# Kernel optimization log

Measured on AMD Instinct MI355X. Metric: run time of the kernel, lower is better.

The kernel has to match this reference:

```python
import jax, jax.numpy as jnp
import numpy as np

N_NODES = 50000
N_EDGES = 1600000
D = 128


def setup_inputs() -> dict:
    key = jax.random.key(0)
    k1, k2, k3, k4 = jax.random.split(key, 4)
    x = jax.random.normal(k1, (N_NODES, D), dtype=jnp.float32)
    edge_index = jax.random.randint(k2, (2, N_EDGES), 0, N_NODES, dtype=jnp.int64)
    # Xavier-uniform-like W; B is zeros in torch init but use small random for grad coverage
    limit = float(np.sqrt(6.0 / (D + D)))
    W = jax.random.uniform(k3, (D, D), dtype=jnp.float32, minval=-limit, maxval=limit)
    B = jax.random.uniform(k4, (D, D), dtype=jnp.float32, minval=-limit, maxval=limit)
    return {"x": x, "edge_index": edge_index, "W": W, "B": B}


def reference(x, edge_index, W, B):
    sources = edge_index[0]
    destinations = edge_index[1]
    # gather messages from source nodes, scatter-add into destinations
    messages = x[sources]  # [E, D]
    aggregated = jax.ops.segment_sum(messages, destinations, num_segments=N_NODES)  # [N, D]
    deg = jax.ops.segment_sum(jnp.ones((N_EDGES,), dtype=x.dtype), destinations, num_segments=N_NODES)
    deg = jnp.where(deg == 0, jnp.asarray(1.0, dtype=x.dtype), deg)
    mean_msg = aggregated / deg[:, None]
    # update: messages @ W.T + x @ B.T
    return mean_msg @ W.T + x @ B.T
```

## Files before the change

kernel.cpp:

```cpp
#include <hip/hip_runtime.h>
#include <hip/hip_bf16.h>

#define NN 50000
#define NE 1600000
#define DD 128
#define NPB 64
#define NBK 782
#define MAXB 2560
#define CHUNK 6144
#define NCB 261
#define WS 136

typedef __attribute__((ext_vector_type(8))) short short8;
typedef __attribute__((ext_vector_type(4))) float f32x4;

__device__ inline unsigned short to_bf16(float v) {
    __hip_bfloat16 h = __float2bfloat16(v);
    return __builtin_bit_cast(unsigned short, h);
}

__global__ __launch_bounds__(1024) void convscatter_k(const int* __restrict__ ei,
                                                      const float* __restrict__ x,
                                                      unsigned int* __restrict__ xb,
                                                      int* __restrict__ gcursor,
                                                      int* __restrict__ ebuf) {
    __shared__ int stg[CHUNK];
    __shared__ int h[NBK];
    __shared__ int lbase[NBK];
    __shared__ int gb[NBK];
    __shared__ int hcur[NBK];
    __shared__ int wsum[16], wbase[16];
    const int t = threadIdx.x;
    const int lane = t & 63, wv = t >> 6;
    const int e0 = blockIdx.x * CHUNK;
    const int ec = min(CHUNK, NE - e0);

    for (int i = t; i < NBK; i += 1024) h[i] = 0;
    __syncthreads();

    unsigned int w2[6];
    #pragma unroll
    for (int u = 0; u < 6; ++u) {
        int i = u * 1024 + t;
        if (i < ec) {
            int src = ei[e0 + i];
            int dst = ei[NE + e0 + i];
            int b = dst >> 6;
            w2[u] = ((unsigned)b << 22) | ((unsigned)src << 6) | (unsigned)(dst & 63);
            atomicAdd(&h[b], 1);
        } else w2[u] = 0xFFFFFFFFu;
    }

    {
        int gid = blockIdx.x * 1024 + t;
        const int total4 = NN * DD / 4;
        for (int i = gid; i < total4; i += NCB * 1024) {
            float4 v = ((const float4*)x)[i];
            int p = __builtin_amdgcn_cvt_pk_fp8_f32(v.x, v.y, 0, false);
            p = __builtin_amdgcn_cvt_pk_fp8_f32(v.z, v.w, p, true);
            xb[i] = (unsigned)p;
        }
    }
    __syncthreads();

    int v = (t < NBK) ? h[t] : 0;
    int s = v;
    #pragma unroll
    for (int o = 1; o < 64; o <<= 1) {
        int u = __shfl_up(s, o);
        if (lane >= o) s += u;
    }
    if (lane == 63) wsum[wv] = s;
    __syncthreads();
    if (wv == 0 && lane < 16) {
        int bv = wsum[lane];
        int bs = bv;
        #pragma unroll
        for (int o = 1; o < 16; o <<= 1) {
            int u = __shfl_up(bs, o);
            if (lane >= o) bs += u;
        }
        wbase[lane] = bs - bv;
    }
    __syncthreads();
    if (t < NBK) {
        int excl = s - v + wbase[wv];
        lbase[t] = excl;
        hcur[t] = excl;
        gb[t] = v ? t * MAXB + atomicAdd(&gcursor[t], v) : 0;
    }
    __syncthreads();

    #pragma unroll
    for (int u = 0; u < 6; ++u) {
        if (w2[u] != 0xFFFFFFFFu) {
            int b = w2[u] >> 22;
            int pos = atomicAdd(&hcur[b], 1);
            stg[pos] = (int)w2[u];
        }
    }
    __syncthreads();

    for (int i = t; i < ec; i += 1024) {
        unsigned int w = (unsigned)stg[i];
        int b = w >> 22;
        ebuf[gb[b] + (i - lbase[b])] = (int)(w & 0x3FFFFFu);
    }
}

__global__ __launch_bounds__(512) void sortagg_k(const unsigned int* __restrict__ xb,
                                                 const int* __restrict__ ebuf,
                                                 const int* __restrict__ gcursor,
                                                 unsigned int* __restrict__ meanb) {
    __shared__ int stg[MAXB];
    __shared__ unsigned short srt[MAXB];
    __shared__ int cnt8[8][NPB];
    __shared__ int cur[NPB], off[NPB + 1];
    const int b = blockIdx.x, t = threadIdx.x;
    const int wv = t >> 6, lane = t & 63;
    const int n = gcursor[b];
    const int* __restrict__ slab = ebuf + (size_t)b * MAXB;
    for (int i = t; i < n; i += 512) stg[i] = slab[i];
    if (lane < NPB) cnt8[wv][lane] = 0;
    __syncthreads();
    for (int i = t; i < n; i += 512) atomicAdd(&cnt8[wv][stg[i] & 63], 1);
    __syncthreads();
    if (t < 64) {
        int v = 0;
        #pragma unroll
        for (int w = 0; w < 8; ++w) v += cnt8[w][t];
        int s = v;
        #pragma unroll
        for (int o = 1; o < 64; o <<= 1) {
            int u = __shfl_up(s, o);
            if (t >= o) s += u;
        }
        cur[t] = s - v;
        off[t] = s - v;
        if (t == 63) off[64] = s;
    }
    __syncthreads();
    for (int i = t; i < n; i += 512) {
        int w = stg[i];
        int pos = atomicAdd(&cur[w & 63], 1);
        srt[pos] = (unsigned short)(w >> 6);
    }
    __syncthreads();

    const int half = lane >> 5, il = lane & 31;
    #pragma unroll
    for (int q = 0; q < 8; ++q) {
        int ln = wv + q * 8;
        int s0 = off[ln], s1 = off[ln + 1];
        float a0 = 0.f, a1 = 0.f, a2 = 0.f, a3 = 0.f;
        int i = s0;
        for (; i + 32 <= s1; i += 32) {
            unsigned int u[16];
            #pragma unroll
            for (int k = 0; k < 16; ++k)
                u[k] = xb[(size_t)srt[i + 2 * k + half] * 32 + il];
            #pragma unroll
            for (int k = 0; k < 16; ++k) {
                auto lo = __builtin_amdgcn_cvt_pk_f32_fp8((int)u[k], false);
                auto hi = __builtin_amdgcn_cvt_pk_f32_fp8((int)u[k], true);
                a0 += lo[0]; a1 += lo[1]; a2 += hi[0]; a3 += hi[1];
            }
        }
        if (i + 16 <= s1) {
            unsigned int u[8];
            #pragma unroll
            for (int k = 0; k < 8; ++k)
                u[k] = xb[(size_t)srt[i + 2 * k + half] * 32 + il];
            #pragma unroll
            for (int k = 0; k < 8; ++k) {
                auto lo = __builtin_amdgcn_cvt_pk_f32_fp8((int)u[k], false);
                auto hi = __builtin_amdgcn_cvt_pk_f32_fp8((int)u[k], true);
                a0 += lo[0]; a1 += lo[1]; a2 += hi[0]; a3 += hi[1];
            }
            i += 16;
        }
        for (; i < s1; i += 2) {
            int e = i + half;
            unsigned int u = (e < s1) ? xb[(size_t)srt[e] * 32 + il] : 0u;
            auto lo = __builtin_amdgcn_cvt_pk_f32_fp8((int)u, false);
            auto hi = __builtin_amdgcn_cvt_pk_f32_fp8((int)u, true);
            a0 += lo[0]; a1 += lo[1]; a2 += hi[0]; a3 += hi[1];
        }
        a0 += __shfl_xor(a0, 32);
        a1 += __shfl_xor(a1, 32);
        a2 += __shfl_xor(a2, 32);
        a3 += __shfl_xor(a3, 32);
        int node = b * NPB + ln;
        if (half == 0 && node < NN) {
            float inv = 1.0f / fmaxf((float)(s1 - s0), 1.0f);
            unsigned lo = (unsigned)to_bf16(a0 * inv) | ((unsigned)to_bf16(a1 * inv) << 16);
            unsigned hi = (unsigned)to_bf16(a2 * inv) | ((unsigned)to_bf16(a3 * inv) << 16);
            ((uint2*)meanb)[(size_t)node * 32 + il] = make_uint2(lo, hi);
        }
    }
}

__global__ __launch_bounds__(256) void gemm_mfma_k(const unsigned short* __restrict__ meanb,
                                                   const float* __restrict__ x,
                                                   const float* __restrict__ W,
                                                   const float* __restrict__ Bm,
                                                   float* __restrict__ out) {
    __shared__ unsigned short Wt[DD * WS];
    __shared__ unsigned short Bt[DD * WS];
    const int tid = threadIdx.x;
    #pragma unroll
    for (int it = 0; it < 16; ++it) {
        int idx = it * 256 + tid;
        int n = idx >> 5;
        int k0 = (idx & 31) * 4;
        float4 w4 = ((const float4*)W)[idx];
        float4 b4 = ((const float4*)Bm)[idx];
        ushort4 wp, bp;
        wp.x = to_bf16(w4.x); wp.y = to_bf16(w4.y); wp.z = to_bf16(w4.z); wp.w = to_bf16(w4.w);
        bp.x = to_bf16(b4.x); bp.y = to_bf16(b4.y); bp.z = to_bf16(b4.z); bp.w = to_bf16(b4.w);
        *(ushort4*)&Wt[n * WS + k0] = wp;
        *(ushort4*)&Bt[n * WS + k0] = bp;
    }
    __syncthreads();

    const int wave = tid >> 6;
    const int lane = tid & 63;
    const int m = lane & 15;
    const int quad = lane >> 4;
    const int rowA = min(blockIdx.x * 64 + wave * 16 + m, NN - 1);

    f32x4 acc[8];
    #pragma unroll
    for (int nt = 0; nt < 8; ++nt) acc[nt] = (f32x4){0.f, 0.f, 0.f, 0.f};

    #pragma unroll
    for (int t = 0; t < 4; ++t) {
        const int k8 = t * 32 + quad * 8;
        short8 mf = *(const short8*)&meanb[(size_t)rowA * DD + k8];
        float xv[8];
        {
            const float4* xq = (const float4*)&x[(size_t)rowA * DD + k8];
            float4 b0 = xq[0], b1 = xq[1];
            xv[0] = b0.x; xv[1] = b0.y; xv[2] = b0.z; xv[3] = b0.w;
            xv[4] = b1.x; xv[5] = b1.y; xv[6] = b1.z; xv[7] = b1.w;
        }
        short8 xh, xl;
        #pragma unroll
        for (int j = 0; j < 8; ++j) {
            unsigned short g = to_bf16(xv[j]);
            xh[j] = (short)g;
            xl[j] = (short)to_bf16(xv[j] - __uint_as_float((unsigned)g << 16));
        }
        #pragma unroll
        for (int nt = 0; nt < 8; ++nt) {
            int nrow = nt * 16 + m;
            short8 wf = *(const short8*)&Wt[nrow * WS + k8];
            short8 bf = *(const short8*)&Bt[nrow * WS + k8];
            acc[nt] = __builtin_amdgcn_mfma_f32_16x16x32_bf16(xl, bf, acc[nt], 0, 0, 0);
            acc[nt] = __builtin_amdgcn_mfma_f32_16x16x32_bf16(mf, wf, acc[nt], 0, 0, 0);
            acc[nt] = __builtin_amdgcn_mfma_f32_16x16x32_bf16(xh, bf, acc[nt], 0, 0, 0);
        }
    }

    const int rowD0 = blockIdx.x * 64 + wave * 16 + quad * 4;
    #pragma unroll
    for (int nt = 0; nt < 8; ++nt) {
        #pragma unroll
        for (int r = 0; r < 4; ++r) {
            int row = rowD0 + r;
            if (row < NN) out[(size_t)row * DD + nt * 16 + m] = acc[nt][r];
        }
    }
}

extern "C" void kernel_launch(void* const* d_in, const int* in_sizes, int n_in,
                              void* d_out, int out_size, void* d_ws, size_t ws_size,
                              hipStream_t stream) {
    const float* x  = (const float*)d_in[0];
    const int*   ei = (const int*)d_in[1];
    const float* W  = (const float*)d_in[2];
    const float* Bm = (const float*)d_in[3];
    float* out = (float*)d_out;

    unsigned int* meanb = (unsigned int*)d_ws;
    unsigned int* xb    = meanb + (size_t)NN * 64;
    int* ebuf     = (int*)(xb + (size_t)NN * 32);
    int* gcursor  = ebuf + (size_t)NBK * MAXB;

    hipMemsetAsync(gcursor, 0, NBK * sizeof(int), stream);
    convscatter_k<<<NCB, 1024, 0, stream>>>(ei, x, xb, gcursor, ebuf);
    sortagg_k<<<NBK, 512, 0, stream>>>(xb, ebuf, gcursor, meanb);
    gemm_mfma_k<<<(NN + 63) / 64, 256, 0, stream>>>((const unsigned short*)meanb, x, W, Bm, out);
}
```

Baseline: 154.0 us.

## Fuse mean aggregation with MFMA GEMM and precompute bf16 weights in scatter

Merges the aggregation and GEMM kernels so each 64-node block keeps its bf16 mean rows in shared memory and runs the MFMA update directly, removing the meanb global round trip and one launch. W and B are converted to bf16 once in the scatter kernel and read from global (L2) by the fused kernel instead of each GEMM block converting them into LDS. The scatter kernel is retuned to 512 blocks of 512 threads with 2 buckets per thread in the scan, and the 32-edge unrolled gather loop is dropped. Risks include more LDS per block in the fused kernel lowering occupancy, and B/W fragment loads from global instead of LDS.

Measured after the change: 177.5 us. 15.3% more time.

```diff
diff --git a/kernel.cpp b/kernel.cpp
--- a/kernel.cpp
+++ b/kernel.cpp
@@ -7,9 +7,9 @@
 #define NPB 64
 #define NBK 782
 #define MAXB 2560
-#define CHUNK 6144
-#define NCB 261
-#define WS 136
+#define CHUNK 3125
+#define NCB 512
+#define MS 136
 
 typedef __attribute__((ext_vector_type(8))) short short8;
 typedef __attribute__((ext_vector_type(4))) float f32x4;
@@ -19,30 +19,33 @@
     return __builtin_bit_cast(unsigned short, h);
 }
 
-__global__ __launch_bounds__(1024) void convscatter_k(const int* __restrict__ ei,
-                                                      const float* __restrict__ x,
-                                                      unsigned int* __restrict__ xb,
-                                                      int* __restrict__ gcursor,
-                                                      int* __restrict__ ebuf) {
+__global__ __launch_bounds__(512) void convscatter_k(const int* __restrict__ ei,
+                                                     const float* __restrict__ x,
+                                                     const float* __restrict__ W,
+                                                     const float* __restrict__ Bm,
+                                                     unsigned int* __restrict__ xb,
+                                                     unsigned int* __restrict__ Wb,
+                                                     unsigned int* __restrict__ Bb,
+                                                     int* __restrict__ gcursor,
+                                                     int* __restrict__ ebuf) {
     __shared__ int stg[CHUNK];
     __shared__ int h[NBK];
     __shared__ int lbase[NBK];
     __shared__ int gb[NBK];
     __shared__ int hcur[NBK];
-    __shared__ int wsum[16], wbase[16];
+    __shared__ int wsum[8], wbase[8];
     const int t = threadIdx.x;
     const int lane = t & 63, wv = t >> 6;
     const int e0 = blockIdx.x * CHUNK;
-    const int ec = min(CHUNK, NE - e0);
-
-    for (int i = t; i < NBK; i += 1024) h[i] = 0;
-    __syncthreads();
-
-    unsigned int w2[6];
-    #pragma unroll
-    for (int u = 0; u < 6; ++u) {
-        int i = u * 1024 + t;
-        if (i < ec) {
+
+    for (int i = t; i < NBK; i += 512) h[i] = 0;
+    __syncthreads();
+
+    unsigned int w2[7];
+    #pragma unroll
+    for (int u = 0; u < 7; ++u) {
+        int i = u * 512 + t;
+        if (i < CHUNK) {
             int src = ei[e0 + i];
             int dst = ei[NE + e0 + i];
             int b = dst >> 6;
@@ -52,19 +55,30 @@
     }
 
     {
-        int gid = blockIdx.x * 1024 + t;
+        int gid = blockIdx.x * 512 + t;
         const int total4 = NN * DD / 4;
-        for (int i = gid; i < total4; i += NCB * 1024) {
+        for (int i = gid; i < total4; i += NCB * 512) {
             float4 v = ((const float4*)x)[i];
             int p = __builtin_amdgcn_cvt_pk_fp8_f32(v.x, v.y, 0, false);
             p = __builtin_amdgcn_cvt_pk_fp8_f32(v.z, v.w, p, true);
             xb[i] = (unsigned)p;
         }
-    }
-    __syncthreads();
-
-    int v = (t < NBK) ? h[t] : 0;
-    int s = v;
+        if (gid < 16384) {
+            if (gid < 8192) {
+                float2 w = ((const float2*)W)[gid];
+                Wb[gid] = (unsigned)to_bf16(w.x) | ((unsigned)to_bf16(w.y) << 16);
+            } else {
+                float2 b = ((const float2*)Bm)[gid - 8192];
+                Bb[gid - 8192] = (unsigned)to_bf16(b.x) | ((unsigned)to_bf16(b.y) << 16);
+            }
+        }
+    }
+    __syncthreads();
+
+    int b0 = 2 * t, b1 = b0 + 1;
+    int h0 = (b0 < NBK) ? h[b0] : 0;
+    int h1 = (b1 < NBK) ? h[b1] : 0;
+    int v = h0 + h1, s = v;
     #pragma unroll
     for (int o = 1; o < 64; o <<= 1) {
         int u = __shfl_up(s, o);
@@ -72,27 +86,31 @@
     }
     if (lane == 63) wsum[wv] = s;
     __syncthreads();
-    if (wv == 0 && lane < 16) {
-        int bv = wsum[lane];
-        int bs = bv;
-        #pragma unroll
-        for (int o = 1; o < 16; o <<= 1) {
+    if (wv == 0 && lane < 8) {
+        int bv = wsum[lane], bs = bv;
+        #pragma unroll
+        for (int o = 1; o < 8; o <<= 1) {
             int u = __shfl_up(bs, o);
             if (lane >= o) bs += u;
         }
         wbase[lane] = bs - bv;
     }
     __syncthreads();
-    if (t < NBK) {
+    {
         int excl = s - v + wbase[wv];
-        lbase[t] = excl;
-        hcur[t] = excl;
-        gb[t] = v ? t * MAXB + atomicAdd(&gcursor[t], v) : 0;
-    }
-    __syncthreads();
-
-    #pragma unroll
-    for (int u = 0; u < 6; ++u) {
+        if (b0 < NBK) {
+            lbase[b0] = excl; hcur[b0] = excl;
+            gb[b0] = h0 ? b0 * MAXB + atomicAdd(&gcursor[b0], h0) : 0;
+        }
+        if (b1 < NBK) {
+            lbase[b1] = excl + h0; hcur[b1] = excl + h0;
+            gb[b1] = h1 ? b1 * MAXB + atomicAdd(&gcursor[b1], h1) : 0;
+        }
+    }
+    __syncthreads();
+
+    #pragma unroll
+    for (int u = 0; u < 7; ++u) {
         if (w2[u] != 0xFFFFFFFFu) {
             int b = w2[u] >> 22;
             int pos = atomicAdd(&hcur[b], 1);
@@ -101,19 +119,23 @@
     }
     __syncthreads();
 
-    for (int i = t; i < ec; i += 1024) {
+    for (int i = t; i < CHUNK; i += 512) {
         unsigned int w = (unsigned)stg[i];
         int b = w >> 22;
         ebuf[gb[b] + (i - lbase[b])] = (int)(w & 0x3FFFFFu);
     }
 }
 
-__global__ __launch_bounds__(512) void sortagg_k(const unsigned int* __restrict__ xb,
-                                                 const int* __restrict__ ebuf,
-                                                 const int* __restrict__ gcursor,
-                                                 unsigned int* __restrict__ meanb) {
+__global__ __launch_bounds__(512) void aggemm_k(const unsigned int* __restrict__ xb,
+                                                const float* __restrict__ x,
+                                                const unsigned short* __restrict__ Wb,
+                                                const unsigned short* __restrict__ Bb,
+                                                const int* __restrict__ ebuf,
+                                                const int* __restrict__ gcursor,
+                                                float* __restrict__ out) {
     __shared__ int stg[MAXB];
     __shared__ unsigned short srt[MAXB];
+    __shared__ unsigned short meanT[NPB * MS];
     __shared__ int cnt8[8][NPB];
     __shared__ int cur[NPB], off[NPB + 1];
     const int b = blockIdx.x, t = threadIdx.x;
@@ -154,19 +176,7 @@
         int s0 = off[ln], s1 = off[ln + 1];
         float a0 = 0.f, a1 = 0.f, a2 = 0.f, a3 = 0.f;
         int i = s0;
-        for (; i + 32 <= s1; i += 32) {
-            unsigned int u[16];
-            #pragma unroll
-            for (int k = 0; k < 16; ++k)
-                u[k] = xb[(size_t)srt[i + 2 * k + half] * 32 + il];
-            #pragma unroll
-            for (int k = 0; k < 16; ++k) {
-                auto lo = __builtin_amdgcn_cvt_pk_f32_fp8((int)u[k], false);
-                auto hi = __builtin_amdgcn_cvt_pk_f32_fp8((int)u[k], true);
-                a0 += lo[0]; a1 += lo[1]; a2 += hi[0]; a3 += hi[1];
-            }
-        }
-        if (i + 16 <= s1) {
+        for (; i + 16 <= s1; i += 16) {
             unsigned int u[8];
             #pragma unroll
             for (int k = 0; k < 8; ++k)
@@ -177,7 +187,6 @@
                 auto hi = __builtin_amdgcn_cvt_pk_f32_fp8((int)u[k], true);
                 a0 += lo[0]; a1 += lo[1]; a2 += hi[0]; a3 += hi[1];
             }
-            i += 16;
         }
         for (; i < s1; i += 2) {
             int e = i + half;
@@ -190,59 +199,35 @@
         a1 += __shfl_xor(a1, 32);
         a2 += __shfl_xor(a2, 32);
         a3 += __shfl_xor(a3, 32);
-        int node = b * NPB + ln;
-        if (half == 0 && node < NN) {
+        if (half == 0) {
             float inv = 1.0f / fmaxf((float)(s1 - s0), 1.0f);
-            unsigned lo = (unsigned)to_bf16(a0 * inv) | ((unsigned)to_bf16(a1 * inv) << 16);
-            unsigned hi = (unsigned)to_bf16(a2 * inv) | ((unsigned)to_bf16(a3 * inv) << 16);
-            ((uint2*)meanb)[(size_t)node * 32 + il] = make_uint2(lo, hi);
-        }
-    }
-}
-
-__global__ __launch_bounds__(256) void gemm_mfma_k(const unsigned short* __restrict__ meanb,
-                                                   const float* __restrict__ x,
-                                                   const float* __restrict__ W,
-                                                   const float* __restrict__ Bm,
-                                                   float* __restrict__ out) {
-    __shared__ unsigned short Wt[DD * WS];
-    __shared__ unsigned short Bt[DD * WS];
-    const int tid = threadIdx.x;
-    #pragma unroll
-    for (int it = 0; it < 16; ++it) {
-        int idx = it * 256 + tid;
-        int n = idx >> 5;
-        int k0 = (idx & 31) * 4;
-        float4 w4 = ((const float4*)W)[idx];
-        float4 b4 = ((const float4*)Bm)[idx];
-        ushort4 wp, bp;
-        wp.x = to_bf16(w4.x); wp.y = to_bf16(w4.y); wp.z = to_bf16(w4.z); wp.w = to_bf16(w4.w);
-        bp.x = to_bf16(b4.x); bp.y = to_bf16(b4.y); bp.z = to_bf16(b4.z); bp.w = to_bf16(b4.w);
-        *(ushort4*)&Wt[n * WS + k0] = wp;
-        *(ushort4*)&Bt[n * WS + k0] = bp;
-    }
-    __syncthreads();
-
-    const int wave = tid >> 6;
-    const int lane = tid & 63;
-    const int m = lane & 15;
-    const int quad = lane >> 4;
-    const int rowA = min(blockIdx.x * 64 + wave * 16 + m, NN - 1);
-
-    f32x4 acc[8];
-    #pragma unroll
-    for (int nt = 0; nt < 8; ++nt) acc[nt] = (f32x4){0.f, 0.f, 0.f, 0.f};
-
-    #pragma unroll
-    for (int t = 0; t < 4; ++t) {
-        const int k8 = t * 32 + quad * 8;
-        short8 mf = *(const short8*)&meanb[(size_t)rowA * DD + k8];
+            ushort4 mp;
+            mp.x = to_bf16(a0 * inv); mp.y = to_bf16(a1 * inv);
+            mp.z = to_bf16(a2 * inv); mp.w = to_bf16(a3 * inv);
+            *(ushort4*)&meanT[ln * MS + il * 4] = mp;
+        }
+    }
+    __syncthreads();
+
+    const int m = lane & 15, quad = lane >> 4;
+    const int rt = wv >> 1, nh = wv & 1;
+    const int bb = b * NPB;
+    const int rowA = min(bb + rt * 16 + m, NN - 1);
+
+    f32x4 acc[4];
+    #pragma unroll
+    for (int nt = 0; nt < 4; ++nt) acc[nt] = (f32x4){0.f, 0.f, 0.f, 0.f};
+
+    #pragma unroll
+    for (int kt = 0; kt < 4; ++kt) {
+        const int k8 = kt * 32 + quad * 8;
+        short8 mf = *(const short8*)&meanT[(rt * 16 + m) * MS + k8];
         float xv[8];
         {
             const float4* xq = (const float4*)&x[(size_t)rowA * DD + k8];
-            float4 b0 = xq[0], b1 = xq[1];
-            xv[0] = b0.x; xv[1] = b0.y; xv[2] = b0.z; xv[3] = b0.w;
-            xv[4] = b1.x; xv[5] = b1.y; xv[6] = b1.z; xv[7] = b1.w;
+            float4 c0 = xq[0], c1 = xq[1];
+            xv[0] = c0.x; xv[1] = c0.y; xv[2] = c0.z; xv[3] = c0.w;
+            xv[4] = c1.x; xv[5] = c1.y; xv[6] = c1.z; xv[7] = c1.w;
         }
         short8 xh, xl;
         #pragma unroll
@@ -252,23 +237,23 @@
             xl[j] = (short)to_bf16(xv[j] - __uint_as_float((unsigned)g << 16));
         }
         #pragma unroll
-        for (int nt = 0; nt < 8; ++nt) {
-            int nrow = nt * 16 + m;
-            short8 wf = *(const short8*)&Wt[nrow * WS + k8];
-            short8 bf = *(const short8*)&Bt[nrow * WS + k8];
+        for (int nt = 0; nt < 4; ++nt) {
+            int nrow = (nh * 4 + nt) * 16 + m;
+            short8 wf = *(const short8*)&Wb[nrow * DD + k8];
+            short8 bf = *(const short8*)&Bb[nrow * DD + k8];
             acc[nt] = __builtin_amdgcn_mfma_f32_16x16x32_bf16(xl, bf, acc[nt], 0, 0, 0);
             acc[nt] = __builtin_amdgcn_mfma_f32_16x16x32_bf16(mf, wf, acc[nt], 0, 0, 0);
             acc[nt] = __builtin_amdgcn_mfma_f32_16x16x32_bf16(xh, bf, acc[nt], 0, 0, 0);
         }
     }
 
-    const int rowD0 = blockIdx.x * 64 + wave * 16 + quad * 4;
-    #pragma unroll
-    for (int nt = 0; nt < 8; ++nt) {
+    const int rowD0 = bb + rt * 16 + quad * 4;
+    #pragma unroll
+    for (int nt = 0; nt < 4; ++nt) {
         #pragma unroll
         for (int r = 0; r < 4; ++r) {
             int row = rowD0 + r;
-            if (row < NN) out[(size_t)row * DD + nt * 16 + m] = acc[nt][r];
+            if (row < NN) out[(size_t)row * DD + (nh * 4 + nt) * 16 + m] = acc[nt][r];
         }
     }
 }
@@ -282,13 +267,14 @@
     const float* Bm = (const float*)d_in[3];
     float* out = (float*)d_out;
 
-    unsigned int* meanb = (unsigned int*)d_ws;
-    unsigned int* xb    = meanb + (size_t)NN * 64;
-    int* ebuf     = (int*)(xb + (size_t)NN * 32);
-    int* gcursor  = ebuf + (size_t)NBK * MAXB;
+    unsigned int* xb = (unsigned int*)d_ws;
+    unsigned int* Wb = xb + (size_t)NN * 32;
+    unsigned int* Bb = Wb + 8192;
+    int* ebuf    = (int*)(Bb + 8192);
+    int* gcursor = ebuf + (size_t)NBK * MAXB;
 
     hipMemsetAsync(gcursor, 0, NBK * sizeof(int), stream);
-    convscatter_k<<<NCB, 1024, 0, stream>>>(ei, x, xb, gcursor, ebuf);
-    sortagg_k<<<NBK, 512, 0, stream>>>(xb, ebuf, gcursor, meanb);
-    gemm_mfma_k<<<(NN + 63) / 64, 256, 0, stream>>>((const unsigned short*)meanb, x, W, Bm, out);
-}
+    convscatter_k<<<NCB, 512, 0, stream>>>(ei, x, W, Bm, xb, Wb, Bb, gcursor, ebuf);
+    aggemm_k<<<NBK, 512, 0, stream>>>(xb, x, (const unsigned short*)Wb,
+                                      (const unsigned short*)Bb, ebuf, gcursor, out);
+}
```
